# Kernel optimization log

Hardware: AMD Instinct MI355X
Metric: run time of the kernel (lower is better)

Reference implementation:

```python
import jax, jax.numpy as jnp
import numpy as np

N = 4096                 # num nodes
SP, GE, TE = 256, 8, 64  # modality input dims
E = 32                   # embed_dim == hidden_features == out_features
H = 2                    # num_heads
D3 = 3 * E               # combined dim = 96
NEG_SLOPE = 0.2


def setup_inputs() -> dict:
    key = jax.random.key(0)
    ks = iter(jax.random.split(key, 64))
    nrm = lambda shape, s=0.05: jax.random.normal(next(ks), shape, jnp.float32) * s
    inp = {
        "spatial": jax.random.normal(next(ks), (N, SP), jnp.float32),
        "genomic": jax.random.normal(next(ks), (N, GE), jnp.float32),
        "temporal": jax.random.normal(next(ks), (N, TE), jnp.float32),
        "adj_matrix": jax.random.randint(next(ks), (N, N), 0, 2, jnp.int32),
        # modality embedding MLPs (Linear + LayerNorm)
        "sp_w": nrm((SP, E)), "sp_b": jnp.zeros((E,)), "sp_lg": jnp.ones((E,)), "sp_lb": jnp.zeros((E,)),
        "ge_w": nrm((GE, E)), "ge_b": jnp.zeros((E,)), "ge_lg": jnp.ones((E,)), "ge_lb": jnp.zeros((E,)),
        "te_w": nrm((TE, E)), "te_b": jnp.zeros((E,)), "te_lg": jnp.ones((E,)), "te_lb": jnp.zeros((E,)),
        # GAT: W_shared [96 -> H*E], attention vector a [2E], out_proj [H*E -> E], LayerNorm(E)
        "gat_w": nrm((D3, H * E)), "gat_a": nrm((2 * E,)),
        "gat_ow": nrm((H * E, E)), "gat_ob": jnp.zeros((E,)),
        "gat_lg": jnp.ones((E,)), "gat_lb": jnp.zeros((E,)),
        # MultiheadAttention (embed 96): packed qkv in_proj and out_proj
        "mha_iw": nrm((D3, 3 * D3)), "mha_ib": jnp.zeros((3 * D3,)),
        "mha_ow": nrm((D3, D3)), "mha_ob": jnp.zeros((D3,)),
        # motor tower
        "m1_w": nrm((D3, 2 * E)), "m1_b": jnp.zeros((2 * E,)), "m1_lg": jnp.ones((2 * E,)), "m1_lb": jnp.zeros((2 * E,)),
        "m2_w": nrm((2 * E, E)), "m2_b": jnp.zeros((E,)), "m2_lg": jnp.ones((E,)), "m2_lb": jnp.zeros((E,)),
        "m3_w": nrm((E, 1)), "m3_b": jnp.zeros((1,)),
        # cognitive tower
        "c1_w": nrm((D3, 2 * E)), "c1_b": jnp.zeros((2 * E,)), "c1_lg": jnp.ones((2 * E,)), "c1_lb": jnp.zeros((2 * E,)),
        "c2_w": nrm((2 * E, E)), "c2_b": jnp.zeros((E,)), "c2_lg": jnp.ones((E,)), "c2_lb": jnp.zeros((E,)),
        "c3_w": nrm((E, 1)), "c3_b": jnp.zeros((1,)),
    }
    return inp


def _ln(x, g, b, eps=1e-5):
    m = x.mean(-1, keepdims=True)
    v = ((x - m) ** 2).mean(-1, keepdims=True)
    return (x - m) / jnp.sqrt(v + eps) * g + b


def _embed(x, w, b, lg, lb):
    return jax.nn.relu(_ln(x @ w + b, lg, lb))  # dropout is identity in eval


def _tower(x, w1, b1, lg1, lb1, w2, b2, lg2, lb2, w3, b3):
    h = jax.nn.relu(_ln(x @ w1 + b1, lg1, lb1))
    h = jax.nn.relu(_ln(h @ w2 + b2, lg2, lb2))
    return h @ w3 + b3


def reference(spatial, genomic, temporal, adj_matrix,
              sp_w, sp_b, sp_lg, sp_lb, ge_w, ge_b, ge_lg, ge_lb,
              te_w, te_b, te_lg, te_lb,
              gat_w, gat_a, gat_ow, gat_ob, gat_lg, gat_lb,
              mha_iw, mha_ib, mha_ow, mha_ob,
              m1_w, m1_b, m1_lg, m1_lb, m2_w, m2_b, m2_lg, m2_lb, m3_w, m3_b,
              c1_w, c1_b, c1_lg, c1_lb, c2_w, c2_b, c2_lg, c2_lb, c3_w, c3_b):
    n = spatial.shape[0]
    s_emb = _embed(spatial, sp_w, sp_b, sp_lg, sp_lb)
    g_emb = _embed(genomic, ge_w, ge_b, ge_lg, ge_lb)
    t_emb = _embed(temporal, te_w, te_b, te_lg, te_lb)
    combined = jnp.concatenate([s_emb, g_emb, t_emb], axis=-1)  # [N, 96]

    # --- TaskSpecificGAT ---
    h = (combined @ gat_w).reshape(n, H, E)  # [N, H, E]
    # e[i,j] = leaky_relu(a . [h_i ; h_j]) = leaky_relu((h @ a1)_i + (h @ a2)_j)
    a1, a2 = gat_a[:E], gat_a[E:]
    f1 = jnp.einsum('nhd,d->nh', h, a1)  # source term
    f2 = jnp.einsum('nhd,d->nh', h, a2)  # target term
    e = jax.nn.leaky_relu(f1[:, None, :] + f2[None, :, :], NEG_SLOPE)  # [N, N, H]
    e = jnp.where(adj_matrix[:, :, None] == 0, -jnp.inf, e)
    alpha = jax.nn.softmax(e, axis=1)  # softmax over neighbors j
    h_out = jnp.einsum('ijh,jhd->ihd', alpha, h).reshape(n, H * E)  # [N, 64]
    gat_out = _ln(h_out @ gat_ow + gat_ob, gat_lg, gat_lb)  # [N, 32]

    # gat_expanded = cat([gat_out]*3) -> [N, 96], attn over seq_len=1
    gx = jnp.tile(gat_out, (1, 3))
    # MHA with a single key/query: softmax over one key == 1, so output = out_proj(v)
    v = gx @ mha_iw[:, 2 * D3:] + mha_ib[2 * D3:]
    attn_out = v @ mha_ow + mha_ob

    final = attn_out + combined
    motor = _tower(final, m1_w, m1_b, m1_lg, m1_lb, m2_w, m2_b, m2_lg, m2_lb, m3_w, m3_b)
    cognitive = jax.nn.sigmoid(
        _tower(final, c1_w, c1_b, c1_lg, c1_lb, c2_w, c2_b, c2_lg, c2_lb, c3_w, c3_b))
    return (motor, cognitive)
```

## Files before the change

kernel.cpp:

```cpp
#include <hip/hip_runtime.h>
#include <math.h>

#define NN 4096
#define LOG2E 1.4426950408889634f

typedef short short8 __attribute__((ext_vector_type(8)));
typedef float f32x4 __attribute__((ext_vector_type(4)));

#define OFF_COMB   0u
#define OFF_F1     393216u
#define OFF_F2     401408u
#define OFF_MAXF2  409600u
#define OFF_W2     409616u
#define OFF_B2     412688u
#define OFF_HT     412800u
#define OFF_PART   543872u

__device__ inline unsigned short f2bf(float x) {
  unsigned u = __float_as_uint(x);
  unsigned r = u + 0x7FFFu + ((u >> 16) & 1u);
  return (unsigned short)(r >> 16);
}

__global__ __launch_bounds__(128) void k_embed(
    const float* __restrict__ spatial, const float* __restrict__ genomic,
    const float* __restrict__ temporal,
    const float* __restrict__ sp_w, const float* __restrict__ sp_b,
    const float* __restrict__ sp_lg, const float* __restrict__ sp_lb,
    const float* __restrict__ ge_w, const float* __restrict__ ge_b,
    const float* __restrict__ ge_lg, const float* __restrict__ ge_lb,
    const float* __restrict__ te_w, const float* __restrict__ te_b,
    const float* __restrict__ te_lg, const float* __restrict__ te_lb,
    const float* __restrict__ gat_w, const float* __restrict__ gat_a,
    float* __restrict__ ws)
{
  int row = blockIdx.x;
  int t = threadIdx.x;
  __shared__ float comb[96];
  __shared__ float hbuf[64];

  if (t < 96) {
    int g = t >> 5, c = t & 31;
    float x;
    if (g == 0) {
      const float* in = spatial + (size_t)row * 256;
      float a = sp_b[c];
#pragma unroll 8
      for (int k = 0; k < 256; k++) a = fmaf(in[k], sp_w[k * 32 + c], a);
      x = a;
    } else if (g == 1) {
      const float* in = genomic + (size_t)row * 8;
      float a = ge_b[c];
#pragma unroll
      for (int k = 0; k < 8; k++) a = fmaf(in[k], ge_w[k * 32 + c], a);
      x = a;
    } else {
      const float* in = temporal + (size_t)row * 64;
      float a = te_b[c];
#pragma unroll 8
      for (int k = 0; k < 64; k++) a = fmaf(in[k], te_w[k * 32 + c], a);
      x = a;
    }
    float s1 = x, s2 = x * x;
    for (int m = 1; m < 32; m <<= 1) {
      s1 += __shfl_xor(s1, m, 32);
      s2 += __shfl_xor(s2, m, 32);
    }
    float mean = s1 * (1.f / 32.f);
    float var  = s2 * (1.f / 32.f) - mean * mean;
    float inv  = rsqrtf(var + 1e-5f);
    const float* lg = (g == 0) ? sp_lg : (g == 1) ? ge_lg : te_lg;
    const float* lb = (g == 0) ? sp_lb : (g == 1) ? ge_lb : te_lb;
    float y = (x - mean) * inv * lg[c] + lb[c];
    y = fmaxf(y, 0.f);
    comb[t] = y;
    ws[OFF_COMB + (size_t)row * 96 + t] = y;
  }
  __syncthreads();
  if (t < 64) {
    float a = 0.f;
#pragma unroll 8
    for (int r = 0; r < 96; r++) a = fmaf(comb[r], gat_w[r * 64 + t], a);
    hbuf[t] = a;
    ((unsigned short*)(ws + OFF_HT))[(size_t)t * NN + row] = f2bf(a);
  }
  __syncthreads();
  if (t < 4) {
    int head = t & 1;
    const float* av = gat_a + ((t >> 1) ? 32 : 0);
    float a = 0.f;
#pragma unroll
    for (int d = 0; d < 32; d++) a = fmaf(hbuf[head * 32 + d], av[d], a);
    if ((t >> 1) == 0) ws[OFF_F1 + head * NN + row] = a;
    else               ws[OFF_F2 + head * NN + row] = a;
  }
}

__global__ __launch_bounds__(128) void k_prep(
    const float* __restrict__ mha_iw, const float* __restrict__ mha_ib,
    const float* __restrict__ mha_ow, const float* __restrict__ mha_ob,
    float* __restrict__ ws)
{
  int b = blockIdx.x, t = threadIdx.x;
  if (b < 32) {
    if (t < 96) {
      float a = 0.f;
      for (int r = 0; r < 96; r++) {
        float fw = mha_iw[(b)      * 288 + 192 + r]
                 + mha_iw[(b + 32) * 288 + 192 + r]
                 + mha_iw[(b + 64) * 288 + 192 + r];
        a = fmaf(fw, mha_ow[r * 96 + t], a);
      }
      ws[OFF_W2 + b * 96 + t] = a;
    }
  } else if (b == 32) {
    if (t < 96) {
      float a = mha_ob[t];
      for (int r = 0; r < 96; r++) a = fmaf(mha_ib[192 + r], mha_ow[r * 96 + t], a);
      ws[OFF_B2 + t] = a;
    }
  } else {
    __shared__ float red[128 * 2];
    float m0 = -1e30f, m1 = -1e30f;
    for (int k = t; k < NN; k += 128) {
      m0 = fmaxf(m0, ws[OFF_F2 + k]);
      m1 = fmaxf(m1, ws[OFF_F2 + NN + k]);
    }
    red[t * 2] = m0; red[t * 2 + 1] = m1;
    __syncthreads();
    if (t < 2) {
      float m = -1e30f;
      for (int k = 0; k < 128; k++) m = fmaxf(m, red[k * 2 + t]);
      ws[OFF_MAXF2 + t] = m;
    }
  }
}

__global__ __launch_bounds__(256) void k_gat3(
    const int* __restrict__ adj,
    const unsigned short* __restrict__ hT,
    const float* __restrict__ f1h,
    const float* __restrict__ f2h,
    const float* __restrict__ maxf2,
    float* __restrict__ part,
    float* __restrict__ lpart, int NS)
{
  int t = threadIdx.x;
  int lane = t & 63, wv = t >> 6;
  int quad = lane >> 4, mrow = lane & 15;
  int ib = blockIdx.x * 64 + wv * 16;
  int i_lane = ib + mrow;
  int slice = NN / NS;
  int jb = blockIdx.y * slice;

  float f1v0 = f1h[i_lane];
  float f1v1 = f1h[NN + i_lane];
  float s0 = f1v0 + maxf2[0], s1 = f1v1 + maxf2[1];
  float sh0 = fmaxf(s0, 0.2f * s0);
  float sh1 = fmaxf(s1, 0.2f * s1);
  float c00 = -sh0 * LOG2E;
  float c01 = -sh1 * LOG2E;

  f32x4 acc00 = {0.f, 0.f, 0.f, 0.f};
  f32x4 acc01 = {0.f, 0.f, 0.f, 0.f};
  f32x4 acc10 = {0.f, 0.f, 0.f, 0.f};
  f32x4 acc11 = {0.f, 0.f, 0.f, 0.f};
  float ls0 = 0.f, ls1 = 0.f;

  const int* adjRow = adj + (size_t)i_lane * NN;

#pragma unroll 2
  for (int jc = jb; jc < jb + slice; jc += 32) {
    int jq = jc + quad * 8;
    int4 am0 = *(const int4*)(adjRow + jq);
    int4 am1 = *(const int4*)(adjRow + jq + 4);
    float4 fa = *(const float4*)(f2h + jq);
    float4 fb = *(const float4*)(f2h + jq + 4);
    float4 fc = *(const float4*)(f2h + NN + jq);
    float4 fd = *(const float4*)(f2h + NN + jq + 4);
    short8 b00 = *(const short8*)(hT + (size_t)(mrow)      * NN + jq);
    short8 b01 = *(const short8*)(hT + (size_t)(16 + mrow) * NN + jq);
    short8 b10 = *(const short8*)(hT + (size_t)(32 + mrow) * NN + jq);
    short8 b11 = *(const short8*)(hT + (size_t)(48 + mrow) * NN + jq);

    float f2a[8] = {fa.x, fa.y, fa.z, fa.w, fb.x, fb.y, fb.z, fb.w};
    float f2b[8] = {fc.x, fc.y, fc.z, fc.w, fd.x, fd.y, fd.z, fd.w};
    int   amv[8] = {am0.x, am0.y, am0.z, am0.w, am1.x, am1.y, am1.z, am1.w};

    union { short8 v; unsigned short u[8]; } a0, a1;
#pragma unroll
    for (int k = 0; k < 8; k++) {
      float e0 = f1v0 + f2a[k];
      float le0 = fmaxf(e0, 0.2f * e0);
      float w0 = __builtin_amdgcn_exp2f(fmaf(le0, LOG2E, c00));
      float e1 = f1v1 + f2b[k];
      float le1 = fmaxf(e1, 0.2f * e1);
      float w1 = __builtin_amdgcn_exp2f(fmaf(le1, LOG2E, c01));
      w0 = amv[k] ? w0 : 0.f;
      w1 = amv[k] ? w1 : 0.f;
      ls0 += w0; ls1 += w1;
      a0.u[k] = f2bf(w0);
      a1.u[k] = f2bf(w1);
    }
    acc00 = __builtin_amdgcn_mfma_f32_16x16x32_bf16(a0.v, b00, acc00, 0, 0, 0);
    acc01 = __builtin_amdgcn_mfma_f32_16x16x32_bf16(a0.v, b01, acc01, 0, 0, 0);
    acc10 = __builtin_amdgcn_mfma_f32_16x16x32_bf16(a1.v, b10, acc10, 0, 0, 0);
    acc11 = __builtin_amdgcn_mfma_f32_16x16x32_bf16(a1.v, b11, acc11, 0, 0, 0);
  }

  ls0 += __shfl_xor(ls0, 16); ls0 += __shfl_xor(ls0, 32);
  ls1 += __shfl_xor(ls1, 16); ls1 += __shfl_xor(ls1, 32);

  int slot = blockIdx.y;
#pragma unroll
  for (int r = 0; r < 4; r++) {
    int ig = ib + quad * 4 + r;
    float* p = part + ((size_t)(slot * NN + ig)) * 64;
    p[mrow]      = acc00[r];
    p[16 + mrow] = acc01[r];
    p[32 + mrow] = acc10[r];
    p[48 + mrow] = acc11[r];
  }
  if (lane < 16) {
    int ig = ib + lane;
    lpart[(size_t)(slot * NN + ig) * 2]     = ls0;
    lpart[(size_t)(slot * NN + ig) * 2 + 1] = ls1;
  }
}

__global__ __launch_bounds__(128) void k_post2(
    const float* __restrict__ gat_ow, const float* __restrict__ gat_ob,
    const float* __restrict__ gat_lg, const float* __restrict__ gat_lb,
    const float* __restrict__ m1_w, const float* __restrict__ m1_b,
    const float* __restrict__ m1_lg, const float* __restrict__ m1_lb,
    const float* __restrict__ m2_w, const float* __restrict__ m2_b,
    const float* __restrict__ m2_lg, const float* __restrict__ m2_lb,
    const float* __restrict__ m3_w, const float* __restrict__ m3_b,
    const float* __restrict__ c1_w, const float* __restrict__ c1_b,
    const float* __restrict__ c1_lg, const float* __restrict__ c1_lb,
    const float* __restrict__ c2_w, const float* __restrict__ c2_b,
    const float* __restrict__ c2_lg, const float* __restrict__ c2_lb,
    const float* __restrict__ c3_w, const float* __restrict__ c3_b,
    const float* __restrict__ part, const float* __restrict__ lpart,
    const float* __restrict__ comb, const float* __restrict__ W2,
    const float* __restrict__ B2,
    float* __restrict__ out, int NS)
{
  int t = threadIdx.x;
  int w = t >> 6, l = t & 63;
  int i = blockIdx.x * 2 + w;
  int slots = NS;

  __shared__ float sh_h[2][64];
  __shared__ float sh_go[2][32];
  __shared__ float sh_fin[2][96];
  __shared__ float sh_t1[2][2][64];

  float a = 0.f;
  for (int s = 0; s < slots; s++) a += part[((size_t)(s * NN + i)) * 64 + l];
  float l0 = 0.f, l1 = 0.f;
  for (int s = 0; s < slots; s++) {
    l0 += lpart[(size_t)(s * NN + i) * 2];
    l1 += lpart[(size_t)(s * NN + i) * 2 + 1];
  }
  sh_h[w][l] = a / (l < 32 ? l0 : l1);
  __syncthreads();

  if (l < 32) {
    float acc = gat_ob[l];
    for (int r = 0; r < 64; r++) acc = fmaf(sh_h[w][r], gat_ow[r * 32 + l], acc);
    float s1 = acc, s2 = acc * acc;
    for (int m = 1; m < 32; m <<= 1) {
      s1 += __shfl_xor(s1, m, 32);
      s2 += __shfl_xor(s2, m, 32);
    }
    float mean = s1 * (1.f / 32.f), var = s2 * (1.f / 32.f) - mean * mean;
    sh_go[w][l] = (acc - mean) * rsqrtf(var + 1e-5f) * gat_lg[l] + gat_lb[l];
  }
  __syncthreads();

  {
    float accA = B2[l];
    for (int d = 0; d < 32; d++) accA = fmaf(sh_go[w][d], W2[d * 96 + l], accA);
    sh_fin[w][l] = accA + comb[(size_t)i * 96 + l];
    if (l < 32) {
      float accB = B2[64 + l];
      for (int d = 0; d < 32; d++) accB = fmaf(sh_go[w][d], W2[d * 96 + 64 + l], accB);
      sh_fin[w][64 + l] = accB + comb[(size_t)i * 96 + 64 + l];
    }
  }
  __syncthreads();

  {
    float am = m1_b[l], ac = c1_b[l];
    for (int r = 0; r < 96; r++) {
      float f = sh_fin[w][r];
      am = fmaf(f, m1_w[r * 64 + l], am);
      ac = fmaf(f, c1_w[r * 64 + l], ac);
    }
    float s1 = am, s2 = am * am;
    for (int m = 1; m < 64; m <<= 1) { s1 += __shfl_xor(s1, m); s2 += __shfl_xor(s2, m); }
    float mean = s1 * (1.f / 64.f), var = s2 * (1.f / 64.f) - mean * mean;
    sh_t1[w][0][l] = fmaxf((am - mean) * rsqrtf(var + 1e-5f) * m1_lg[l] + m1_lb[l], 0.f);
    s1 = ac; s2 = ac * ac;
    for (int m = 1; m < 64; m <<= 1) { s1 += __shfl_xor(s1, m); s2 += __shfl_xor(s2, m); }
    mean = s1 * (1.f / 64.f); var = s2 * (1.f / 64.f) - mean * mean;
    sh_t1[w][1][l] = fmaxf((ac - mean) * rsqrtf(var + 1e-5f) * c1_lg[l] + c1_lb[l], 0.f);
  }
  __syncthreads();

  {
    int tw = l >> 5, c = l & 31;
    const float* w2  = tw ? c2_w  : m2_w;
    const float* b2  = tw ? c2_b  : m2_b;
    const float* lg2 = tw ? c2_lg : m2_lg;
    const float* lb2 = tw ? c2_lb : m2_lb;
    float a2 = b2[c];
    for (int r = 0; r < 64; r++) a2 = fmaf(sh_t1[w][tw][r], w2[r * 32 + c], a2);
    float u1 = a2, u2 = a2 * a2;
    for (int m = 1; m < 32; m <<= 1) {
      u1 += __shfl_xor(u1, m, 32);
      u2 += __shfl_xor(u2, m, 32);
    }
    float mean = u1 * (1.f / 32.f), var = u2 * (1.f / 32.f) - mean * mean;
    float y2 = fmaxf((a2 - mean) * rsqrtf(var + 1e-5f) * lg2[c] + lb2[c], 0.f);
    float p = y2 * (tw ? c3_w[c] : m3_w[c]);
    for (int m = 1; m < 32; m <<= 1) p += __shfl_xor(p, m, 32);
    if (c == 0) {
      float v = p + (tw ? c3_b[0] : m3_b[0]);
      if (tw) out[NN + i] = 1.f / (1.f + expf(-v));
      else    out[i] = v;
    }
  }
}

extern "C" void kernel_launch(void* const* d_in, const int* in_sizes, int n_in,
                              void* d_out, int out_size, void* d_ws, size_t ws_size,
                              hipStream_t stream) {
  (void)in_sizes; (void)n_in; (void)out_size;
  const float* spatial  = (const float*)d_in[0];
  const float* genomic  = (const float*)d_in[1];
  const float* temporal = (const float*)d_in[2];
  const int*   adj      = (const int*)d_in[3];
  const float* sp_w = (const float*)d_in[4];
  const float* sp_b = (const float*)d_in[5];
  const float* sp_lg = (const float*)d_in[6];
  const float* sp_lb = (const float*)d_in[7];
  const float* ge_w = (const float*)d_in[8];
  const float* ge_b = (const float*)d_in[9];
  const float* ge_lg = (const float*)d_in[10];
  const float* ge_lb = (const float*)d_in[11];
  const float* te_w = (const float*)d_in[12];
  const float* te_b = (const float*)d_in[13];
  const float* te_lg = (const float*)d_in[14];
  const float* te_lb = (const float*)d_in[15];
  const float* gat_w = (const float*)d_in[16];
  const float* gat_a = (const float*)d_in[17];
  const float* gat_ow = (const float*)d_in[18];
  const float* gat_ob = (const float*)d_in[19];
  const float* gat_lg = (const float*)d_in[20];
  const float* gat_lb = (const float*)d_in[21];
  const float* mha_iw = (const float*)d_in[22];
  const float* mha_ib = (const float*)d_in[23];
  const float* mha_ow = (const float*)d_in[24];
  const float* mha_ob = (const float*)d_in[25];
  const float* m1_w = (const float*)d_in[26];
  const float* m1_b = (const float*)d_in[27];
  const float* m1_lg = (const float*)d_in[28];
  const float* m1_lb = (const float*)d_in[29];
  const float* m2_w = (const float*)d_in[30];
  const float* m2_b = (const float*)d_in[31];
  const float* m2_lg = (const float*)d_in[32];
  const float* m2_lb = (const float*)d_in[33];
  const float* m3_w = (const float*)d_in[34];
  const float* m3_b = (const float*)d_in[35];
  const float* c1_w = (const float*)d_in[36];
  const float* c1_b = (const float*)d_in[37];
  const float* c1_lg = (const float*)d_in[38];
  const float* c1_lb = (const float*)d_in[39];
  const float* c2_w = (const float*)d_in[40];
  const float* c2_b = (const float*)d_in[41];
  const float* c2_lg = (const float*)d_in[42];
  const float* c2_lb = (const float*)d_in[43];
  const float* c3_w = (const float*)d_in[44];
  const float* c3_b = (const float*)d_in[45];

  float* ws  = (float*)d_ws;
  float* out = (float*)d_out;

  int NS = 8;
  while (NS > 1) {
    size_t need = (size_t)(OFF_PART + (size_t)NS * NN * 64 + (size_t)NS * NN * 2) * 4;
    if (need <= ws_size) break;
    NS >>= 1;
  }
  float* part  = ws + OFF_PART;
  float* lpart = part + (size_t)NS * NN * 64;

  k_embed<<<NN, 128, 0, stream>>>(spatial, genomic, temporal,
                                  sp_w, sp_b, sp_lg, sp_lb,
                                  ge_w, ge_b, ge_lg, ge_lb,
                                  te_w, te_b, te_lg, te_lb,
                                  gat_w, gat_a, ws);
  k_prep<<<34, 128, 0, stream>>>(mha_iw, mha_ib, mha_ow, mha_ob, ws);
  dim3 g2(NN / 64, NS);
  k_gat3<<<g2, 256, 0, stream>>>(adj,
                                 (const unsigned short*)(ws + OFF_HT),
                                 ws + OFF_F1, ws + OFF_F2, ws + OFF_MAXF2,
                                 part, lpart, NS);
  k_post2<<<NN / 2, 128, 0, stream>>>(gat_ow, gat_ob, gat_lg, gat_lb,
                                      m1_w, m1_b, m1_lg, m1_lb,
                                      m2_w, m2_b, m2_lg, m2_lb,
                                      m3_w, m3_b,
                                      c1_w, c1_b, c1_lg, c1_lb,
                                      c2_w, c2_b, c2_lg, c2_lb,
                                      c3_w, c3_b,
                                      part, lpart, ws + OFF_COMB,
                                      ws + OFF_W2, ws + OFF_B2,
                                      out, NS);
}
```

Measured before the change: 261.5 us.

## Fuse embedding and prep into tiled 64-row kernel with atomic max of f2

Replaces the per-row embedding kernel and the separate prep kernel with one kernel. Each block stages 64 rows of inputs in shared memory and computes the modality linears, LayerNorms and the GAT projection as register-tiled matmuls. One extra block builds the fused MHA weight, and the global max of f2 is reduced with an order-preserving atomicMax after a memset, which removes a kernel launch and a serial reduction. It also raises the j-split count of the GAT kernel from 8 to 16 to give it more blocks, at the cost of larger partial buffers and more post-reduction work. The embed grid is small (65 blocks), which may leave much of the GPU idle.

```diff
diff --git a/kernel.cpp b/kernel.cpp
--- a/kernel.cpp
+++ b/kernel.cpp
@@ -21,8 +21,21 @@
   unsigned r = u + 0x7FFFu + ((u >> 16) & 1u);
   return (unsigned short)(r >> 16);
 }
-
-__global__ __launch_bounds__(128) void k_embed(
+__device__ inline unsigned fenc(float f) {
+  unsigned b = __float_as_uint(f);
+  return (b & 0x80000000u) ? ~b : (b | 0x80000000u);
+}
+__device__ inline float fdec(unsigned e) {
+  return __uint_as_float((e & 0x80000000u) ? (e ^ 0x80000000u) : ~e);
+}
+
+#define XS 258
+#define TS 66
+#define GS 12
+#define CS 98
+#define HS 67
+
+__global__ __launch_bounds__(256) void k_embed2(
     const float* __restrict__ spatial, const float* __restrict__ genomic,
     const float* __restrict__ temporal,
     const float* __restrict__ sp_w, const float* __restrict__ sp_b,
@@ -32,106 +45,195 @@
     const float* __restrict__ te_w, const float* __restrict__ te_b,
     const float* __restrict__ te_lg, const float* __restrict__ te_lb,
     const float* __restrict__ gat_w, const float* __restrict__ gat_a,
-    float* __restrict__ ws)
-{
-  int row = blockIdx.x;
-  int t = threadIdx.x;
-  __shared__ float comb[96];
-  __shared__ float hbuf[64];
-
-  if (t < 96) {
-    int g = t >> 5, c = t & 31;
-    float x;
-    if (g == 0) {
-      const float* in = spatial + (size_t)row * 256;
-      float a = sp_b[c];
-#pragma unroll 8
-      for (int k = 0; k < 256; k++) a = fmaf(in[k], sp_w[k * 32 + c], a);
-      x = a;
-    } else if (g == 1) {
-      const float* in = genomic + (size_t)row * 8;
-      float a = ge_b[c];
-#pragma unroll
-      for (int k = 0; k < 8; k++) a = fmaf(in[k], ge_w[k * 32 + c], a);
-      x = a;
-    } else {
-      const float* in = temporal + (size_t)row * 64;
-      float a = te_b[c];
-#pragma unroll 8
-      for (int k = 0; k < 64; k++) a = fmaf(in[k], te_w[k * 32 + c], a);
-      x = a;
-    }
-    float s1 = x, s2 = x * x;
-    for (int m = 1; m < 32; m <<= 1) {
-      s1 += __shfl_xor(s1, m, 32);
-      s2 += __shfl_xor(s2, m, 32);
-    }
-    float mean = s1 * (1.f / 32.f);
-    float var  = s2 * (1.f / 32.f) - mean * mean;
-    float inv  = rsqrtf(var + 1e-5f);
-    const float* lg = (g == 0) ? sp_lg : (g == 1) ? ge_lg : te_lg;
-    const float* lb = (g == 0) ? sp_lb : (g == 1) ? ge_lb : te_lb;
-    float y = (x - mean) * inv * lg[c] + lb[c];
-    y = fmaxf(y, 0.f);
-    comb[t] = y;
-    ws[OFF_COMB + (size_t)row * 96 + t] = y;
-  }
-  __syncthreads();
-  if (t < 64) {
-    float a = 0.f;
-#pragma unroll 8
-    for (int r = 0; r < 96; r++) a = fmaf(comb[r], gat_w[r * 64 + t], a);
-    hbuf[t] = a;
-    ((unsigned short*)(ws + OFF_HT))[(size_t)t * NN + row] = f2bf(a);
-  }
-  __syncthreads();
-  if (t < 4) {
-    int head = t & 1;
-    const float* av = gat_a + ((t >> 1) ? 32 : 0);
-    float a = 0.f;
-#pragma unroll
-    for (int d = 0; d < 32; d++) a = fmaf(hbuf[head * 32 + d], av[d], a);
-    if ((t >> 1) == 0) ws[OFF_F1 + head * NN + row] = a;
-    else               ws[OFF_F2 + head * NN + row] = a;
-  }
-}
-
-__global__ __launch_bounds__(128) void k_prep(
     const float* __restrict__ mha_iw, const float* __restrict__ mha_ib,
     const float* __restrict__ mha_ow, const float* __restrict__ mha_ob,
     float* __restrict__ ws)
 {
-  int b = blockIdx.x, t = threadIdx.x;
-  if (b < 32) {
-    if (t < 96) {
-      float a = 0.f;
-      for (int r = 0; r < 96; r++) {
-        float fw = mha_iw[(b)      * 288 + 192 + r]
-                 + mha_iw[(b + 32) * 288 + 192 + r]
-                 + mha_iw[(b + 64) * 288 + 192 + r];
-        a = fmaf(fw, mha_ow[r * 96 + t], a);
-      }
-      ws[OFF_W2 + b * 96 + t] = a;
-    }
-  } else if (b == 32) {
+  __shared__ float x_s[64][XS];
+  __shared__ float t_s[64][TS];
+  __shared__ float g_s[64][GS];
+  __shared__ float c_s[64][CS];
+  __shared__ float h_s[64][HS];
+
+  int t = threadIdx.x;
+  int blk = blockIdx.x;
+
+  if (blk == 64) {
+    float* fw_s = &x_s[0][0];
+    float* ow_s = fw_s + 32 * 97;
+    for (int idx = t; idx < 3072; idx += 256) {
+      int b = idx / 96, r = idx - b * 96;
+      fw_s[b * 97 + r] = mha_iw[b * 288 + 192 + r]
+                       + mha_iw[(b + 32) * 288 + 192 + r]
+                       + mha_iw[(b + 64) * 288 + 192 + r];
+    }
+    for (int idx = t; idx < 9216; idx += 256) {
+      int r = idx / 96, col = idx - r * 96;
+      ow_s[r * 97 + col] = mha_ow[idx];
+    }
     if (t < 96) {
       float a = mha_ob[t];
       for (int r = 0; r < 96; r++) a = fmaf(mha_ib[192 + r], mha_ow[r * 96 + t], a);
       ws[OFF_B2 + t] = a;
     }
-  } else {
-    __shared__ float red[128 * 2];
-    float m0 = -1e30f, m1 = -1e30f;
-    for (int k = t; k < NN; k += 128) {
-      m0 = fmaxf(m0, ws[OFF_F2 + k]);
-      m1 = fmaxf(m1, ws[OFF_F2 + NN + k]);
-    }
-    red[t * 2] = m0; red[t * 2 + 1] = m1;
     __syncthreads();
-    if (t < 2) {
-      float m = -1e30f;
-      for (int k = 0; k < 128; k++) m = fmaxf(m, red[k * 2 + t]);
-      ws[OFF_MAXF2 + t] = m;
+    int lane = t & 63, wv = t >> 6;
+    int b = lane & 31, half = lane >> 5;
+    int cb = (wv * 2 + half) * 12;
+    float acc[12];
+#pragma unroll
+    for (int m = 0; m < 12; m++) acc[m] = 0.f;
+    for (int r = 0; r < 96; r++) {
+      float fv = fw_s[b * 97 + r];
+#pragma unroll
+      for (int m = 0; m < 12; m++) acc[m] = fmaf(fv, ow_s[r * 97 + cb + m], acc[m]);
+    }
+#pragma unroll
+    for (int m = 0; m < 12; m++) ws[OFF_W2 + b * 96 + cb + m] = acc[m];
+    return;
+  }
+
+  int row0 = blk * 64;
+  int lane = t & 63, wv = t >> 6;
+
+  {
+    const float2* xsrc = (const float2*)(spatial + (size_t)row0 * 256);
+    for (int idx = t; idx < 64 * 128; idx += 256) {
+      float2 v = xsrc[idx];
+      int r = idx >> 7, c2 = idx & 127;
+      *(float2*)&x_s[r][c2 * 2] = v;
+    }
+    const float2* tsrc = (const float2*)(temporal + (size_t)row0 * 64);
+    for (int idx = t; idx < 64 * 32; idx += 256) {
+      float2 v = tsrc[idx];
+      int r = idx >> 5, c2 = idx & 31;
+      *(float2*)&t_s[r][c2 * 2] = v;
+    }
+    const float2* gsrc = (const float2*)(genomic + (size_t)row0 * 8);
+    for (int idx = t; idx < 64 * 4; idx += 256) {
+      float2 v = gsrc[idx];
+      int r = idx >> 2, c2 = idx & 3;
+      *(float2*)&g_s[r][c2 * 2] = v;
+    }
+  }
+  __syncthreads();
+
+  int cs = __builtin_amdgcn_readfirstlane(wv * 8);
+  {
+    float acc[8];
+#pragma unroll
+    for (int m = 0; m < 8; m++) acc[m] = sp_b[cs + m];
+#pragma unroll 4
+    for (int k = 0; k < 256; k += 2) {
+      float2 xv = *(const float2*)&x_s[lane][k];
+#pragma unroll
+      for (int m = 0; m < 8; m++) {
+        acc[m] = fmaf(xv.x, sp_w[k * 32 + cs + m], acc[m]);
+        acc[m] = fmaf(xv.y, sp_w[(k + 1) * 32 + cs + m], acc[m]);
+      }
+    }
+#pragma unroll
+    for (int m = 0; m < 8; m++) c_s[lane][cs + m] = acc[m];
+  }
+  {
+    float acc[8];
+#pragma unroll
+    for (int m = 0; m < 8; m++) acc[m] = ge_b[cs + m];
+#pragma unroll
+    for (int k = 0; k < 8; k += 2) {
+      float2 xv = *(const float2*)&g_s[lane][k];
+#pragma unroll
+      for (int m = 0; m < 8; m++) {
+        acc[m] = fmaf(xv.x, ge_w[k * 32 + cs + m], acc[m]);
+        acc[m] = fmaf(xv.y, ge_w[(k + 1) * 32 + cs + m], acc[m]);
+      }
+    }
+#pragma unroll
+    for (int m = 0; m < 8; m++) c_s[lane][32 + cs + m] = acc[m];
+  }
+  {
+    float acc[8];
+#pragma unroll
+    for (int m = 0; m < 8; m++) acc[m] = te_b[cs + m];
+#pragma unroll 4
+    for (int k = 0; k < 64; k += 2) {
+      float2 xv = *(const float2*)&t_s[lane][k];
+#pragma unroll
+      for (int m = 0; m < 8; m++) {
+        acc[m] = fmaf(xv.x, te_w[k * 32 + cs + m], acc[m]);
+        acc[m] = fmaf(xv.y, te_w[(k + 1) * 32 + cs + m], acc[m]);
+      }
+    }
+#pragma unroll
+    for (int m = 0; m < 8; m++) c_s[lane][64 + cs + m] = acc[m];
+  }
+  __syncthreads();
+
+  {
+    int c = t & 31, j = t >> 5;
+    for (int idx = j; idx < 192; idx += 8) {
+      int r = idx & 63, grp = idx >> 6;
+      float x = c_s[r][grp * 32 + c];
+      float s1 = x, s2 = x * x;
+      for (int m = 1; m < 32; m <<= 1) {
+        s1 += __shfl_xor(s1, m, 32);
+        s2 += __shfl_xor(s2, m, 32);
+      }
+      float mean = s1 * (1.f / 32.f);
+      float var  = s2 * (1.f / 32.f) - mean * mean;
+      float inv  = rsqrtf(var + 1e-5f);
+      const float* lg = (grp == 0) ? sp_lg : (grp == 1) ? ge_lg : te_lg;
+      const float* lb = (grp == 0) ? sp_lb : (grp == 1) ? ge_lb : te_lb;
+      float y = fmaxf((x - mean) * inv * lg[c] + lb[c], 0.f);
+      c_s[r][grp * 32 + c] = y;
+      ws[OFF_COMB + (size_t)(row0 + r) * 96 + grp * 32 + c] = y;
+    }
+  }
+  __syncthreads();
+
+  {
+    int cs2 = __builtin_amdgcn_readfirstlane(wv * 16);
+    float acc[16];
+#pragma unroll
+    for (int m = 0; m < 16; m++) acc[m] = 0.f;
+#pragma unroll 2
+    for (int k = 0; k < 96; k += 2) {
+      float2 cv = *(const float2*)&c_s[lane][k];
+#pragma unroll
+      for (int m = 0; m < 16; m++) {
+        acc[m] = fmaf(cv.x, gat_w[k * 64 + cs2 + m], acc[m]);
+        acc[m] = fmaf(cv.y, gat_w[(k + 1) * 64 + cs2 + m], acc[m]);
+      }
+    }
+#pragma unroll
+    for (int m = 0; m < 16; m++) h_s[lane][cs2 + m] = acc[m];
+  }
+  __syncthreads();
+
+  {
+    unsigned short* hT = (unsigned short*)(ws + OFF_HT);
+    int j = t & 63, dg = t >> 6;
+#pragma unroll
+    for (int dd = 0; dd < 16; dd++) {
+      int d = dg * 16 + dd;
+      hT[(size_t)d * NN + row0 + j] = f2bf(h_s[j][d]);
+    }
+  }
+  {
+    int r = t & 63, q = t >> 6;
+    int head = q & 1, isf2 = q >> 1;
+    const float* av = gat_a + (isf2 ? 32 : 0);
+    float a = 0.f;
+#pragma unroll
+    for (int d = 0; d < 32; d++) a = fmaf(h_s[r][head * 32 + d], av[d], a);
+    if (!isf2) {
+      ws[OFF_F1 + head * NN + row0 + r] = a;
+    } else {
+      ws[OFF_F2 + head * NN + row0 + r] = a;
+      float mx = a;
+      for (int m = 1; m < 64; m <<= 1) mx = fmaxf(mx, __shfl_xor(mx, m));
+      if (r == 0)
+        atomicMax(((unsigned*)(ws + OFF_MAXF2)) + head, fenc(mx));
     }
   }
 }
@@ -141,7 +243,7 @@
     const unsigned short* __restrict__ hT,
     const float* __restrict__ f1h,
     const float* __restrict__ f2h,
-    const float* __restrict__ maxf2,
+    const unsigned* __restrict__ maxf2,
     float* __restrict__ part,
     float* __restrict__ lpart, int NS)
 {
@@ -155,7 +257,7 @@
 
   float f1v0 = f1h[i_lane];
   float f1v1 = f1h[NN + i_lane];
-  float s0 = f1v0 + maxf2[0], s1 = f1v1 + maxf2[1];
+  float s0 = f1v0 + fdec(maxf2[0]), s1 = f1v1 + fdec(maxf2[1]);
   float sh0 = fmaxf(s0, 0.2f * s0);
   float sh1 = fmaxf(s1, 0.2f * s1);
   float c00 = -sh0 * LOG2E;
@@ -388,7 +490,7 @@
   float* ws  = (float*)d_ws;
   float* out = (float*)d_out;
 
-  int NS = 8;
+  int NS = 16;
   while (NS > 1) {
     size_t need = (size_t)(OFF_PART + (size_t)NS * NN * 64 + (size_t)NS * NN * 2) * 4;
     if (need <= ws_size) break;
@@ -397,16 +499,19 @@
   float* part  = ws + OFF_PART;
   float* lpart = part + (size_t)NS * NN * 64;
 
-  k_embed<<<NN, 128, 0, stream>>>(spatial, genomic, temporal,
-                                  sp_w, sp_b, sp_lg, sp_lb,
-                                  ge_w, ge_b, ge_lg, ge_lb,
-                                  te_w, te_b, te_lg, te_lb,
-                                  gat_w, gat_a, ws);
-  k_prep<<<34, 128, 0, stream>>>(mha_iw, mha_ib, mha_ow, mha_ob, ws);
+  hipMemsetAsync((char*)d_ws + (size_t)OFF_MAXF2 * 4, 0, 16, stream);
+
+  k_embed2<<<65, 256, 0, stream>>>(spatial, genomic, temporal,
+                                   sp_w, sp_b, sp_lg, sp_lb,
+                                   ge_w, ge_b, ge_lg, ge_lb,
+                                   te_w, te_b, te_lg, te_lb,
+                                   gat_w, gat_a,
+                                   mha_iw, mha_ib, mha_ow, mha_ob, ws);
   dim3 g2(NN / 64, NS);
   k_gat3<<<g2, 256, 0, stream>>>(adj,
                                  (const unsigned short*)(ws + OFF_HT),
-                                 ws + OFF_F1, ws + OFF_F2, ws + OFF_MAXF2,
+                                 ws + OFF_F1, ws + OFF_F2,
+                                 (const unsigned*)(ws + OFF_MAXF2),
                                  part, lpart, NS);
   k_post2<<<NN / 2, 128, 0, stream>>>(gat_ow, gat_ob, gat_lg, gat_lb,
                                       m1_w, m1_b, m1_lg, m1_lb,
```

Result: slower. 289.3 us (+10.6%).

## Split embed stage into parallel kernels, double GAT slices, reorganize partial layout

Applied to the files above, without the earlier changes.

The per-row embed kernel is replaced by three kernels. k_comb runs one 32-lane group per (row, modality) with float4 input loads and also holds the MHA weight folding. k_proj computes the GAT projection for four rows per block and writes packed bf16 transposed values. k_max is a single-block max reduction over f2. The number of GAT column slices goes from 8 to 16 for more blocks. Partial sums are stored row-major per node so k_post2, now handling four nodes per block with unrolled loops, reads them contiguously. The post kernel hardcodes 16 slices, so if the workspace forces a smaller NS it would read the wrong data.

```diff
diff --git a/kernel.cpp b/kernel.cpp
--- a/kernel.cpp
+++ b/kernel.cpp
@@ -22,7 +22,7 @@
   return (unsigned short)(r >> 16);
 }
 
-__global__ __launch_bounds__(128) void k_embed(
+__global__ __launch_bounds__(256) void k_comb(
     const float* __restrict__ spatial, const float* __restrict__ genomic,
     const float* __restrict__ temporal,
     const float* __restrict__ sp_w, const float* __restrict__ sp_b,
@@ -31,108 +31,168 @@
     const float* __restrict__ ge_lg, const float* __restrict__ ge_lb,
     const float* __restrict__ te_w, const float* __restrict__ te_b,
     const float* __restrict__ te_lg, const float* __restrict__ te_lb,
-    const float* __restrict__ gat_w, const float* __restrict__ gat_a,
-    float* __restrict__ ws)
-{
-  int row = blockIdx.x;
-  int t = threadIdx.x;
-  __shared__ float comb[96];
-  __shared__ float hbuf[64];
-
-  if (t < 96) {
-    int g = t >> 5, c = t & 31;
-    float x;
-    if (g == 0) {
-      const float* in = spatial + (size_t)row * 256;
-      float a = sp_b[c];
-#pragma unroll 8
-      for (int k = 0; k < 256; k++) a = fmaf(in[k], sp_w[k * 32 + c], a);
-      x = a;
-    } else if (g == 1) {
-      const float* in = genomic + (size_t)row * 8;
-      float a = ge_b[c];
-#pragma unroll
-      for (int k = 0; k < 8; k++) a = fmaf(in[k], ge_w[k * 32 + c], a);
-      x = a;
-    } else {
-      const float* in = temporal + (size_t)row * 64;
-      float a = te_b[c];
-#pragma unroll 8
-      for (int k = 0; k < 64; k++) a = fmaf(in[k], te_w[k * 32 + c], a);
-      x = a;
-    }
-    float s1 = x, s2 = x * x;
-    for (int m = 1; m < 32; m <<= 1) {
-      s1 += __shfl_xor(s1, m, 32);
-      s2 += __shfl_xor(s2, m, 32);
-    }
-    float mean = s1 * (1.f / 32.f);
-    float var  = s2 * (1.f / 32.f) - mean * mean;
-    float inv  = rsqrtf(var + 1e-5f);
-    const float* lg = (g == 0) ? sp_lg : (g == 1) ? ge_lg : te_lg;
-    const float* lb = (g == 0) ? sp_lb : (g == 1) ? ge_lb : te_lb;
-    float y = (x - mean) * inv * lg[c] + lb[c];
-    y = fmaxf(y, 0.f);
-    comb[t] = y;
-    ws[OFF_COMB + (size_t)row * 96 + t] = y;
-  }
-  __syncthreads();
-  if (t < 64) {
-    float a = 0.f;
-#pragma unroll 8
-    for (int r = 0; r < 96; r++) a = fmaf(comb[r], gat_w[r * 64 + t], a);
-    hbuf[t] = a;
-    ((unsigned short*)(ws + OFF_HT))[(size_t)t * NN + row] = f2bf(a);
-  }
-  __syncthreads();
-  if (t < 4) {
-    int head = t & 1;
-    const float* av = gat_a + ((t >> 1) ? 32 : 0);
-    float a = 0.f;
-#pragma unroll
-    for (int d = 0; d < 32; d++) a = fmaf(hbuf[head * 32 + d], av[d], a);
-    if ((t >> 1) == 0) ws[OFF_F1 + head * NN + row] = a;
-    else               ws[OFF_F2 + head * NN + row] = a;
-  }
-}
-
-__global__ __launch_bounds__(128) void k_prep(
     const float* __restrict__ mha_iw, const float* __restrict__ mha_ib,
     const float* __restrict__ mha_ow, const float* __restrict__ mha_ob,
     float* __restrict__ ws)
 {
-  int b = blockIdx.x, t = threadIdx.x;
-  if (b < 32) {
-    if (t < 96) {
-      float a = 0.f;
+  int t = threadIdx.x;
+  int blk = blockIdx.x;
+
+  if (blk >= 1536) {
+    if (blk < 1548) {
+      int idx = (blk - 1536) * 256 + t;
+      int b = idx / 96, col = idx - b * 96;
+      float acc = 0.f;
       for (int r = 0; r < 96; r++) {
-        float fw = mha_iw[(b)      * 288 + 192 + r]
+        float fw = mha_iw[b * 288 + 192 + r]
                  + mha_iw[(b + 32) * 288 + 192 + r]
                  + mha_iw[(b + 64) * 288 + 192 + r];
-        a = fmaf(fw, mha_ow[r * 96 + t], a);
+        acc = fmaf(fw, mha_ow[r * 96 + col], acc);
       }
-      ws[OFF_W2 + b * 96 + t] = a;
-    }
-  } else if (b == 32) {
-    if (t < 96) {
-      float a = mha_ob[t];
-      for (int r = 0; r < 96; r++) a = fmaf(mha_ib[192 + r], mha_ow[r * 96 + t], a);
-      ws[OFF_B2 + t] = a;
-    }
+      ws[OFF_W2 + b * 96 + col] = acc;
+    } else {
+      if (t < 96) {
+        float acc = mha_ob[t];
+        for (int r = 0; r < 96; r++) acc = fmaf(mha_ib[192 + r], mha_ow[r * 96 + t], acc);
+        ws[OFF_B2 + t] = acc;
+      }
+    }
+    return;
+  }
+
+  int j = blk * 8 + (t >> 5);
+  int grp = j >> 12;
+  int row = j & 4095;
+  int c = t & 31;
+
+  float val;
+  const float* lg;
+  const float* lb;
+  if (grp == 0) {
+    const float* in = spatial + (size_t)row * 256;
+    float a0 = 0.f, a1 = 0.f, a2 = 0.f, a3 = 0.f;
+#pragma unroll 4
+    for (int k = 0; k < 256; k += 4) {
+      float4 x = *(const float4*)(in + k);
+      a0 = fmaf(x.x, sp_w[(k)     * 32 + c], a0);
+      a1 = fmaf(x.y, sp_w[(k + 1) * 32 + c], a1);
+      a2 = fmaf(x.z, sp_w[(k + 2) * 32 + c], a2);
+      a3 = fmaf(x.w, sp_w[(k + 3) * 32 + c], a3);
+    }
+    val = sp_b[c] + ((a0 + a1) + (a2 + a3));
+    lg = sp_lg; lb = sp_lb;
+  } else if (grp == 1) {
+    const float* in = genomic + (size_t)row * 8;
+    float4 x0 = *(const float4*)(in);
+    float4 x1 = *(const float4*)(in + 4);
+    float a0 = ge_b[c];
+    a0 = fmaf(x0.x, ge_w[0 * 32 + c], a0);
+    a0 = fmaf(x0.y, ge_w[1 * 32 + c], a0);
+    a0 = fmaf(x0.z, ge_w[2 * 32 + c], a0);
+    a0 = fmaf(x0.w, ge_w[3 * 32 + c], a0);
+    a0 = fmaf(x1.x, ge_w[4 * 32 + c], a0);
+    a0 = fmaf(x1.y, ge_w[5 * 32 + c], a0);
+    a0 = fmaf(x1.z, ge_w[6 * 32 + c], a0);
+    a0 = fmaf(x1.w, ge_w[7 * 32 + c], a0);
+    val = a0;
+    lg = ge_lg; lb = ge_lb;
   } else {
-    __shared__ float red[128 * 2];
-    float m0 = -1e30f, m1 = -1e30f;
-    for (int k = t; k < NN; k += 128) {
-      m0 = fmaxf(m0, ws[OFF_F2 + k]);
-      m1 = fmaxf(m1, ws[OFF_F2 + NN + k]);
-    }
-    red[t * 2] = m0; red[t * 2 + 1] = m1;
-    __syncthreads();
-    if (t < 2) {
-      float m = -1e30f;
-      for (int k = 0; k < 128; k++) m = fmaxf(m, red[k * 2 + t]);
-      ws[OFF_MAXF2 + t] = m;
-    }
+    const float* in = temporal + (size_t)row * 64;
+    float a0 = 0.f, a1 = 0.f, a2 = 0.f, a3 = 0.f;
+#pragma unroll 4
+    for (int k = 0; k < 64; k += 4) {
+      float4 x = *(const float4*)(in + k);
+      a0 = fmaf(x.x, te_w[(k)     * 32 + c], a0);
+      a1 = fmaf(x.y, te_w[(k + 1) * 32 + c], a1);
+      a2 = fmaf(x.z, te_w[(k + 2) * 32 + c], a2);
+      a3 = fmaf(x.w, te_w[(k + 3) * 32 + c], a3);
+    }
+    val = te_b[c] + ((a0 + a1) + (a2 + a3));
+    lg = te_lg; lb = te_lb;
+  }
+
+  float s1 = val, s2 = val * val;
+#pragma unroll
+  for (int m = 1; m < 32; m <<= 1) {
+    s1 += __shfl_xor(s1, m, 32);
+    s2 += __shfl_xor(s2, m, 32);
+  }
+  float mean = s1 * (1.f / 32.f);
+  float var  = s2 * (1.f / 32.f) - mean * mean;
+  float y = fmaxf((val - mean) * rsqrtf(var + 1e-5f) * lg[c] + lb[c], 0.f);
+  ws[OFF_COMB + (size_t)row * 96 + grp * 32 + c] = y;
+}
+
+__global__ __launch_bounds__(256) void k_proj(
+    const float* __restrict__ gat_w, const float* __restrict__ gat_a,
+    float* __restrict__ ws)
+{
+  __shared__ float h_s[4][64];
+  int t = threadIdx.x;
+  int w = t >> 6, d = t & 63;
+  int row0 = blockIdx.x * 4;
+  int row = row0 + w;
+
+  const float* crow = ws + OFF_COMB + (size_t)row * 96;
+  float a0 = 0.f, a1 = 0.f;
+#pragma unroll 8
+  for (int k = 0; k < 96; k += 2) {
+    a0 = fmaf(crow[k],     gat_w[k * 64 + d],       a0);
+    a1 = fmaf(crow[k + 1], gat_w[(k + 1) * 64 + d], a1);
+  }
+  float h = a0 + a1;
+
+  int dc = d & 31;
+  float p1 = h * gat_a[dc];
+  float p2 = h * gat_a[32 + dc];
+#pragma unroll
+  for (int m = 1; m < 32; m <<= 1) {
+    p1 += __shfl_xor(p1, m, 32);
+    p2 += __shfl_xor(p2, m, 32);
+  }
+  if (dc == 0) {
+    int head = d >> 5;
+    ws[OFF_F1 + head * NN + row] = p1;
+    ws[OFF_F2 + head * NN + row] = p2;
+  }
+
+  h_s[w][d] = h;
+  __syncthreads();
+  if (t < 64) {
+    unsigned u0 = (unsigned)f2bf(h_s[0][t]) | ((unsigned)f2bf(h_s[1][t]) << 16);
+    unsigned u1 = (unsigned)f2bf(h_s[2][t]) | ((unsigned)f2bf(h_s[3][t]) << 16);
+    uint2 v; v.x = u0; v.y = u1;
+    unsigned short* hT = (unsigned short*)(ws + OFF_HT);
+    *(uint2*)(hT + (size_t)t * NN + row0) = v;
+  }
+}
+
+__global__ __launch_bounds__(256) void k_max(float* __restrict__ ws)
+{
+  __shared__ float red[4][2];
+  int t = threadIdx.x;
+  const float4* p0 = (const float4*)(ws + OFF_F2);
+  const float4* p1 = (const float4*)(ws + OFF_F2 + NN);
+  float m0 = -1e30f, m1 = -1e30f;
+#pragma unroll
+  for (int q = 0; q < 4; q++) {
+    float4 v0 = p0[t + q * 256];
+    float4 v1 = p1[t + q * 256];
+    m0 = fmaxf(m0, fmaxf(fmaxf(v0.x, v0.y), fmaxf(v0.z, v0.w)));
+    m1 = fmaxf(m1, fmaxf(fmaxf(v1.x, v1.y), fmaxf(v1.z, v1.w)));
+  }
+#pragma unroll
+  for (int m = 1; m < 64; m <<= 1) {
+    m0 = fmaxf(m0, __shfl_xor(m0, m));
+    m1 = fmaxf(m1, __shfl_xor(m1, m));
+  }
+  if ((t & 63) == 0) { red[t >> 6][0] = m0; red[t >> 6][1] = m1; }
+  __syncthreads();
+  if (t == 0) {
+    float r0 = red[0][0], r1 = red[0][1];
+    for (int q = 1; q < 4; q++) { r0 = fmaxf(r0, red[q][0]); r1 = fmaxf(r1, red[q][1]); }
+    ws[OFF_MAXF2] = r0;
+    ws[OFF_MAXF2 + 1] = r1;
   }
 }
 
@@ -215,7 +275,7 @@
 #pragma unroll
   for (int r = 0; r < 4; r++) {
     int ig = ib + quad * 4 + r;
-    float* p = part + ((size_t)(slot * NN + ig)) * 64;
+    float* p = part + (size_t)ig * (NS * 64) + slot * 64;
     p[mrow]      = acc00[r];
     p[16 + mrow] = acc01[r];
     p[32 + mrow] = acc10[r];
@@ -223,12 +283,12 @@
   }
   if (lane < 16) {
     int ig = ib + lane;
-    lpart[(size_t)(slot * NN + ig) * 2]     = ls0;
-    lpart[(size_t)(slot * NN + ig) * 2 + 1] = ls1;
-  }
-}
-
-__global__ __launch_bounds__(128) void k_post2(
+    lpart[((size_t)ig * NS + slot) * 2]     = ls0;
+    lpart[((size_t)ig * NS + slot) * 2 + 1] = ls1;
+  }
+}
+
+__global__ __launch_bounds__(256) void k_post2(
     const float* __restrict__ gat_ow, const float* __restrict__ gat_ob,
     const float* __restrict__ gat_lg, const float* __restrict__ gat_lb,
     const float* __restrict__ m1_w, const float* __restrict__ m1_b,
@@ -248,28 +308,38 @@
 {
   int t = threadIdx.x;
   int w = t >> 6, l = t & 63;
-  int i = blockIdx.x * 2 + w;
-  int slots = NS;
-
-  __shared__ float sh_h[2][64];
-  __shared__ float sh_go[2][32];
-  __shared__ float sh_fin[2][96];
-  __shared__ float sh_t1[2][2][64];
-
-  float a = 0.f;
-  for (int s = 0; s < slots; s++) a += part[((size_t)(s * NN + i)) * 64 + l];
-  float l0 = 0.f, l1 = 0.f;
-  for (int s = 0; s < slots; s++) {
-    l0 += lpart[(size_t)(s * NN + i) * 2];
-    l1 += lpart[(size_t)(s * NN + i) * 2 + 1];
-  }
-  sh_h[w][l] = a / (l < 32 ? l0 : l1);
+  int i = blockIdx.x * 4 + w;
+
+  __shared__ float sh_h[4][64];
+  __shared__ float sh_go[4][32];
+  __shared__ float sh_fin[4][96];
+  __shared__ float sh_t1[4][2][64];
+
+  {
+    const float* pr = part + (size_t)i * (NS * 64);
+    float a0 = 0.f, a1 = 0.f, a2 = 0.f, a3 = 0.f;
+#pragma unroll
+    for (int s = 0; s < 16; s += 4) {
+      a0 += pr[(s)     * 64 + l];
+      a1 += pr[(s + 1) * 64 + l];
+      a2 += pr[(s + 2) * 64 + l];
+      a3 += pr[(s + 3) * 64 + l];
+    }
+    float a = (a0 + a1) + (a2 + a3);
+    const float* lr = lpart + (size_t)i * NS * 2;
+    float l0 = 0.f, l1 = 0.f;
+#pragma unroll
+    for (int s = 0; s < 16; s++) { l0 += lr[s * 2]; l1 += lr[s * 2 + 1]; }
+    sh_h[w][l] = a / (l < 32 ? l0 : l1);
+  }
   __syncthreads();
 
   if (l < 32) {
     float acc = gat_ob[l];
+#pragma unroll 8
     for (int r = 0; r < 64; r++) acc = fmaf(sh_h[w][r], gat_ow[r * 32 + l], acc);
     float s1 = acc, s2 = acc * acc;
+#pragma unroll
     for (int m = 1; m < 32; m <<= 1) {
       s1 += __shfl_xor(s1, m, 32);
       s2 += __shfl_xor(s2, m, 32);
@@ -281,10 +351,12 @@
 
   {
     float accA = B2[l];
+#pragma unroll 8
     for (int d = 0; d < 32; d++) accA = fmaf(sh_go[w][d], W2[d * 96 + l], accA);
     sh_fin[w][l] = accA + comb[(size_t)i * 96 + l];
     if (l < 32) {
       float accB = B2[64 + l];
+#pragma unroll 8
       for (int d = 0; d < 32; d++) accB = fmaf(sh_go[w][d], W2[d * 96 + 64 + l], accB);
       sh_fin[w][64 + l] = accB + comb[(size_t)i * 96 + 64 + l];
     }
@@ -293,16 +365,19 @@
 
   {
     float am = m1_b[l], ac = c1_b[l];
+#pragma unroll 4
     for (int r = 0; r < 96; r++) {
       float f = sh_fin[w][r];
       am = fmaf(f, m1_w[r * 64 + l], am);
       ac = fmaf(f, c1_w[r * 64 + l], ac);
     }
     float s1 = am, s2 = am * am;
+#pragma unroll
     for (int m = 1; m < 64; m <<= 1) { s1 += __shfl_xor(s1, m); s2 += __shfl_xor(s2, m); }
     float mean = s1 * (1.f / 64.f), var = s2 * (1.f / 64.f) - mean * mean;
     sh_t1[w][0][l] = fmaxf((am - mean) * rsqrtf(var + 1e-5f) * m1_lg[l] + m1_lb[l], 0.f);
     s1 = ac; s2 = ac * ac;
+#pragma unroll
     for (int m = 1; m < 64; m <<= 1) { s1 += __shfl_xor(s1, m); s2 += __shfl_xor(s2, m); }
     mean = s1 * (1.f / 64.f); var = s2 * (1.f / 64.f) - mean * mean;
     sh_t1[w][1][l] = fmaxf((ac - mean) * rsqrtf(var + 1e-5f) * c1_lg[l] + c1_lb[l], 0.f);
@@ -316,8 +391,10 @@
     const float* lg2 = tw ? c2_lg : m2_lg;
     const float* lb2 = tw ? c2_lb : m2_lb;
     float a2 = b2[c];
+#pragma unroll 4
     for (int r = 0; r < 64; r++) a2 = fmaf(sh_t1[w][tw][r], w2[r * 32 + c], a2);
     float u1 = a2, u2 = a2 * a2;
+#pragma unroll
     for (int m = 1; m < 32; m <<= 1) {
       u1 += __shfl_xor(u1, m, 32);
       u2 += __shfl_xor(u2, m, 32);
@@ -325,6 +402,7 @@
     float mean = u1 * (1.f / 32.f), var = u2 * (1.f / 32.f) - mean * mean;
     float y2 = fmaxf((a2 - mean) * rsqrtf(var + 1e-5f) * lg2[c] + lb2[c], 0.f);
     float p = y2 * (tw ? c3_w[c] : m3_w[c]);
+#pragma unroll
     for (int m = 1; m < 32; m <<= 1) p += __shfl_xor(p, m, 32);
     if (c == 0) {
       float v = p + (tw ? c3_b[0] : m3_b[0]);
@@ -388,7 +466,7 @@
   float* ws  = (float*)d_ws;
   float* out = (float*)d_out;
 
-  int NS = 8;
+  int NS = 16;
   while (NS > 1) {
     size_t need = (size_t)(OFF_PART + (size_t)NS * NN * 64 + (size_t)NS * NN * 2) * 4;
     if (need <= ws_size) break;
@@ -397,18 +475,19 @@
   float* part  = ws + OFF_PART;
   float* lpart = part + (size_t)NS * NN * 64;
 
-  k_embed<<<NN, 128, 0, stream>>>(spatial, genomic, temporal,
-                                  sp_w, sp_b, sp_lg, sp_lb,
-                                  ge_w, ge_b, ge_lg, ge_lb,
-                                  te_w, te_b, te_lg, te_lb,
-                                  gat_w, gat_a, ws);
-  k_prep<<<34, 128, 0, stream>>>(mha_iw, mha_ib, mha_ow, mha_ob, ws);
+  k_comb<<<1549, 256, 0, stream>>>(spatial, genomic, temporal,
+                                   sp_w, sp_b, sp_lg, sp_lb,
+                                   ge_w, ge_b, ge_lg, ge_lb,
+                                   te_w, te_b, te_lg, te_lb,
+                                   mha_iw, mha_ib, mha_ow, mha_ob, ws);
+  k_proj<<<NN / 4, 256, 0, stream>>>(gat_w, gat_a, ws);
+  k_max<<<1, 256, 0, stream>>>(ws);
   dim3 g2(NN / 64, NS);
   k_gat3<<<g2, 256, 0, stream>>>(adj,
                                  (const unsigned short*)(ws + OFF_HT),
                                  ws + OFF_F1, ws + OFF_F2, ws + OFF_MAXF2,
                                  part, lpart, NS);
-  k_post2<<<NN / 2, 128, 0, stream>>>(gat_ow, gat_ob, gat_lg, gat_lb,
+  k_post2<<<NN / 4, 256, 0, stream>>>(gat_ow, gat_ob, gat_lg, gat_lb,
                                       m1_w, m1_b, m1_lg, m1_lb,
                                       m2_w, m2_b, m2_lg, m2_lb,
                                       m3_w, m3_b,
```

Result: no change. 260.3 us (-0.5%).
